# Kernel optimization log

Measured on AMD Instinct MI355X. Metric: run time of the kernel, lower is better.

The kernel has to match this reference:

```python
import jax, jax.numpy as jnp
import numpy as np

N_EMBED = 384
N_HEAD = 6
HEAD_DIM = N_EMBED // N_HEAD


def setup_inputs() -> dict:
    key = jax.random.key(0)
    k1, k2, k3 = jax.random.split(key, 3)
    B, T = 128, 256
    x = jax.random.normal(k1, (B, T, N_EMBED), dtype=jnp.float32)
    # nn.Linear(N_EMBED, 3*N_EMBED, bias=False): weight [3*N_EMBED, N_EMBED],
    # applied as x @ W.T -> store transposed [N_EMBED, 3*N_EMBED]
    W_qkv = jax.random.normal(k2, (N_EMBED, 3 * N_EMBED), dtype=jnp.float32) * (N_EMBED ** -0.5)
    W_proj = jax.random.normal(k3, (N_EMBED, N_EMBED), dtype=jnp.float32) * (N_EMBED ** -0.5)
    return {"x": x, "W_qkv": W_qkv, "W_proj": W_proj}


def reference(x, W_qkv, W_proj):
    B, T, C = x.shape
    qkv = jnp.einsum('btc,cd->btd', x, W_qkv)  # [B,T,3C]
    q, k, v = jnp.split(qkv, 3, axis=-1)
    # [B, H, T, Dh]
    q = q.reshape(B, T, N_HEAD, HEAD_DIM).transpose(0, 2, 1, 3)
    k = k.reshape(B, T, N_HEAD, HEAD_DIM).transpose(0, 2, 1, 3)
    v = v.reshape(B, T, N_HEAD, HEAD_DIM).transpose(0, 2, 1, 3)
    scale = HEAD_DIM ** -0.5
    wei = jnp.einsum('bhqd,bhkd->bhqk', q, k) * scale  # [B,H,T,T]
    causal = jnp.tril(jnp.ones((T, T), dtype=bool))
    wei = jnp.where(causal[None, None, :, :], wei, -jnp.inf)
    wei = jax.nn.softmax(wei, axis=-1)
    # dropout layers are identity in eval mode
    out = jnp.einsum('bhqk,bhkd->bhqd', wei, v)  # [B,H,T,Dh]
    out = out.transpose(0, 2, 1, 3).reshape(B, T, C)
    out = jnp.einsum('btc,cd->btd', out, W_proj)
    return out
```

## Files before the change

### kernel.cpp

```cpp
#include <hip/hip_runtime.h>
#include <hip/hip_bf16.h>

typedef __attribute__((ext_vector_type(8))) short short8;
typedef __attribute__((ext_vector_type(4))) float f32x4;
typedef __attribute__((ext_vector_type(4))) unsigned short ush4;

typedef const __attribute__((address_space(1))) void* gas_p;
typedef __attribute__((address_space(3))) void* las_p;
#define GLOAD_LDS16(g, l) __builtin_amdgcn_global_load_lds((gas_p)(const void*)(g), (las_p)(void*)(l), 16, 0, 0)

__device__ __forceinline__ unsigned short f2bf(float f) {
    union { float f; unsigned int u; } v; v.f = f;
    unsigned int r = v.u + 0x7FFFu + ((v.u >> 16) & 1u);
    return (unsigned short)(r >> 16);
}
__device__ __forceinline__ unsigned pk2(float a, float b) {
    return (unsigned)f2bf(a) | ((unsigned)f2bf(b) << 16);
}

__global__ __launch_bounds__(256) void cast_all_kernel(
    const float* __restrict__ x, const float* __restrict__ Wqkv, const float* __restrict__ Wproj,
    unsigned short* __restrict__ xb, unsigned short* __restrict__ wqkvt,
    unsigned short* __restrict__ wprojt)
{
    const int bid = blockIdx.x;
    if (bid < 6144) {
        int i = bid * 256 + threadIdx.x;
        const float4* p = (const float4*)x + (size_t)i * 2;
        float4 a = p[0], b = p[1];
        short8 o;
        o[0] = (short)f2bf(a.x); o[1] = (short)f2bf(a.y);
        o[2] = (short)f2bf(a.z); o[3] = (short)f2bf(a.w);
        o[4] = (short)f2bf(b.x); o[5] = (short)f2bf(b.y);
        o[6] = (short)f2bf(b.z); o[7] = (short)f2bf(b.w);
        *(short8*)(xb + (size_t)i * 8) = o;
    } else if (bid < 7872) {
        int idx = (bid - 6144) * 256 + threadIdx.x;
        int n = idx / 384, k = idx - n * 384;
        wqkvt[idx] = f2bf(Wqkv[(size_t)k * 1152 + n]);
    } else {
        int idx = (bid - 7872) * 256 + threadIdx.x;
        int n = idx / 384, k = idx - n * 384;
        wprojt[idx] = f2bf(Wproj[(size_t)k * 384 + n]);
    }
}

template<int MODE, int NP>
__global__ __launch_bounds__(256, 2) void gemm_bt_kernel(
    const unsigned short* __restrict__ A, const unsigned short* __restrict__ Bt,
    void* __restrict__ C0, unsigned short* __restrict__ C1,
    int M, int N, int K)
{
    __shared__ __align__(16) unsigned short Sh[3 * 128 * 64];
    unsigned short* As = Sh;
    const int tid = threadIdx.x;
    const int lane = tid & 63, wv = tid >> 6;
    const int c = lane & 15, g = lane >> 4;
    const int wm = (wv >> 1) * 64, wn = (wv & 1) * 64;

    const int mpx = (M >> 7) >> 3;
    const int id = blockIdx.x, xcd = id & 7, kk = id >> 3;
    const long m0 = (long)(xcd * mpx + kk / NP) * 128;
    const long n0 = (long)(kk % NP) * 128;

    f32x4 acc[4][4] = {};
    const int xr = (c & 7) << 4;

    int chrow[4], chsc[4];
    #pragma unroll
    for (int i = 0; i < 4; ++i) {
        int ch = i * 256 + wv * 64 + lane;
        chrow[i] = ch >> 3;
        chsc[i] = ((ch & 7) ^ (chrow[i] & 7)) * 8;
    }

#define STAGE_A(kt)                                                            \
    {                                                                          \
        _Pragma("unroll")                                                      \
        for (int i = 0; i < 4; ++i)                                            \
            GLOAD_LDS16(&A[(m0 + chrow[i]) * (size_t)K + (kt) + chsc[i]],      \
                        &As[(i * 256 + wv * 64) * 8]);                         \
    }
#define STAGE_B(bufofs, kt)                                                    \
    {                                                                          \
        _Pragma("unroll")                                                      \
        for (int i = 0; i < 4; ++i)                                            \
            GLOAD_LDS16(&Bt[(n0 + chrow[i]) * (size_t)K + (kt) + chsc[i]],     \
                        &Sh[(bufofs) + (i * 256 + wv * 64) * 8]);              \
    }

    STAGE_A(0);
    STAGE_B(8192, 0);
    __syncthreads();

    const int nt = K >> 6;
    for (int t = 0; t < nt; ++t) {
        const int bofs = 8192 + (t & 1) * 8192;
        if (t + 1 < nt) STAGE_B(8192 + ((t + 1) & 1) * 8192, (t + 1) * 64);
        const unsigned short* Bcur = Sh + bofs;
        #pragma unroll
        for (int ks = 0; ks < 2; ++ks) {
            short8 af[4], bf_[4];
            #pragma unroll
            for (int i = 0; i < 4; ++i)
                af[i] = *(const short8*)((char*)As +
                    (((wm + i * 16 + c) * 128 + (ks * 32 + g * 8) * 2) ^ xr));
            #pragma unroll
            for (int i = 0; i < 4; ++i)
                bf_[i] = *(const short8*)((char*)Bcur +
                    (((wn + i * 16 + c) * 128 + (ks * 32 + g * 8) * 2) ^ xr));
            #pragma unroll
            for (int mi = 0; mi < 4; ++mi)
                #pragma unroll
                for (int ni = 0; ni < 4; ++ni)
                    acc[mi][ni] = __builtin_amdgcn_mfma_f32_16x16x32_bf16(
                        af[mi], bf_[ni], acc[mi][ni], 0, 0, 0);
        }
        __syncthreads();
        if (t + 1 < nt) {
            STAGE_A((t + 1) * 64);
            __syncthreads();
        }
    }
#undef STAGE_A
#undef STAGE_B

    if (MODE == 1) {
        #pragma unroll
        for (int mi = 0; mi < 4; ++mi)
            #pragma unroll
            for (int ni = 0; ni < 4; ++ni)
                #pragma unroll
                for (int r = 0; r < 4; ++r) {
                    long m = m0 + wm + mi * 16 + g * 4 + r;
                    long n = n0 + wn + ni * 16 + c;
                    ((float*)C0)[m * N + n] = acc[mi][ni][r];
                }
    } else if (n0 < 768) {
        #pragma unroll
        for (int mi = 0; mi < 4; ++mi)
            #pragma unroll
            for (int ni = 0; ni < 4; ++ni)
                #pragma unroll
                for (int r = 0; r < 4; ++r) {
                    long m = m0 + wm + mi * 16 + g * 4 + r;
                    long n = n0 + wn + ni * 16 + c;
                    ((unsigned short*)C0)[m * 768 + n] = f2bf(acc[mi][ni][r]);
                }
    } else {
        char* wbase = (char*)Sh + wv * 8192;
        #pragma unroll
        for (int ni = 0; ni < 4; ++ni)
            #pragma unroll
            for (int mi = 0; mi < 4; ++mi)
                #pragma unroll
                for (int r = 0; r < 4; ++r) {
                    int d = ni * 16 + c, t = mi * 16 + g * 4 + r;
                    int byte = (d * 128 + t * 2) ^ ((d & 7) << 4);
                    *(unsigned short*)(wbase + byte) = f2bf(acc[mi][ni][r]);
                }
        __asm__ __volatile__("" ::: "memory");
        int h = (int)((n0 + wn - 768) >> 6);
        long b = (m0 + wm) >> 8;
        int t0 = (int)((m0 + wm) & 255);
        long bh = b * 6 + h;
        #pragma unroll
        for (int it = 0; it < 8; ++it) {
            int d = it * 8 + (lane >> 3), ck = lane & 7;
            short8 v = *(const short8*)(wbase + ((d * 128 + ck * 16) ^ ((d & 7) << 4)));
            *(short8*)&C1[(bh * 64 + d) * 256 + t0 + ck * 8] = v;
        }
    }
}

__global__ __launch_bounds__(256, 3) void attn_kernel(
    const unsigned short* __restrict__ qk,
    const unsigned short* __restrict__ vt,
    unsigned short* __restrict__ outp)
{
    const int bh = blockIdx.x;
    const int b = bh / 6, h = bh - b * 6;
    const int tid = threadIdx.x;
    const int lane = tid & 63, wv = tid >> 6;
    const int c = lane & 15, g = lane >> 4;

    __shared__ unsigned short Ks[256 * 64];
    __shared__ unsigned short Pl[4][16 * 64];

    #pragma unroll
    for (int it = 0; it < 8; ++it) {
        int ch = it * 256 + tid;
        int row = ch >> 3, col = (ch & 7) * 8;
        int db = (row * 128 + col * 2) ^ ((row & 7) << 4);
        *(short8*)((char*)Ks + db) =
            *(const short8*)&qk[(size_t)(b * 256 + row) * 768 + 384 + h * 64 + col];
    }
    __syncthreads();

    char* plw = (char*)Pl[wv];

    for (int t = 0; t < 2; ++t) {
        const int p = t ? 7 - wv : wv;
        const int jlast = p >> 1;
        const int modd = (p & 1) * 32;
        const int qt0 = p * 32;

        short8 aq[2][2];
        #pragma unroll
        for (int mi = 0; mi < 2; ++mi)
            #pragma unroll
            for (int ks = 0; ks < 2; ++ks)
                aq[mi][ks] = *(const short8*)&qk[
                    (size_t)(b * 256 + qt0 + mi * 16 + c) * 768 + h * 64 + ks * 32 + g * 8];

        f32x4 o[2][4] = {};
        float mrun[2] = {-1e30f, -1e30f}, lrun[2] = {0.f, 0.f};

        for (int j = 0; j <= jlast; ++j) {
            short8 bv[4][2];
            #pragma unroll
            for (int nd = 0; nd < 4; ++nd)
                #pragma unroll
                for (int ks = 0; ks < 2; ++ks)
                    bv[nd][ks] = *(const short8*)&vt[
                        ((size_t)bh * 64 + nd * 16 + c) * 256 + j * 64 + ks * 32 + g * 8];

            short8 bk[4][2];
            #pragma unroll
            for (int ni = 0; ni < 4; ++ni)
                #pragma unroll
                for (int ks = 0; ks < 2; ++ks) {
                    int key = j * 64 + ni * 16 + c;
                    bk[ni][ks] = *(const short8*)((char*)Ks +
                        ((key * 128 + (ks * 32 + g * 8) * 2) ^ ((key & 7) << 4)));
                }

            #pragma unroll
            for (int mi = 0; mi < 2; ++mi) {
                float pv[4][4];
                #pragma unroll
                for (int ni = 0; ni < 4; ++ni) {
                    f32x4 z = {0.f, 0.f, 0.f, 0.f};
                    z = __builtin_amdgcn_mfma_f32_16x16x32_bf16(bk[ni][0], aq[mi][0], z, 0, 0, 0);
                    z = __builtin_amdgcn_mfma_f32_16x16x32_bf16(bk[ni][1], aq[mi][1], z, 0, 0, 0);
                    #pragma unroll
                    for (int r = 0; r < 4; ++r) {
                        float v = z[r] * 0.125f;
                        if (j == jlast) {
                            int kloc = ni * 16 + g * 4 + r;
                            int qloc = mi * 16 + c + modd;
                            if (kloc > qloc) v = -1e30f;
                        }
                        pv[ni][r] = v;
                    }
                }
                float m01 = fmaxf(fmaxf(pv[0][0], pv[0][1]), fmaxf(pv[0][2], pv[0][3]));
                float m11 = fmaxf(fmaxf(pv[1][0], pv[1][1]), fmaxf(pv[1][2], pv[1][3]));
                float m21 = fmaxf(fmaxf(pv[2][0], pv[2][1]), fmaxf(pv[2][2], pv[2][3]));
                float m31 = fmaxf(fmaxf(pv[3][0], pv[3][1]), fmaxf(pv[3][2], pv[3][3]));
                float m1 = fmaxf(fmaxf(m01, m11), fmaxf(m21, m31));
                m1 = fmaxf(m1, __shfl_xor(m1, 16));
                m1 = fmaxf(m1, __shfl_xor(m1, 32));
                float mold = mrun[mi];
                float mnew = fmaxf(mold, m1);
                float fac = __expf(mold - mnew);
                float ssum = 0.f;
                #pragma unroll
                for (int ni = 0; ni < 4; ++ni)
                    #pragma unroll
                    for (int r = 0; r < 4; ++r) {
                        float pp = __expf(pv[ni][r] - mnew);
                        pv[ni][r] = pp;
                        ssum += pp;
                    }
                ssum += __shfl_xor(ssum, 16);
                ssum += __shfl_xor(ssum, 32);
                lrun[mi] = lrun[mi] * fac + ssum;
                mrun[mi] = mnew;
                #pragma unroll
                for (int nd = 0; nd < 4; ++nd)
                    #pragma unroll
                    for (int r = 0; r < 4; ++r) o[mi][nd][r] *= fac;

                __asm__ __volatile__("" ::: "memory");
                #pragma unroll
                for (int ni = 0; ni < 4; ++ni) {
                    uint2 w;
                    w.x = pk2(pv[ni][0], pv[ni][1]);
                    w.y = pk2(pv[ni][2], pv[ni][3]);
                    *(uint2*)(plw + ((c * 128 + ni * 32 + g * 8) ^ ((c & 7) << 4))) = w;
                }
                __asm__ __volatile__("" ::: "memory");

                short8 ap[2];
                #pragma unroll
                for (int ks = 0; ks < 2; ++ks)
                    ap[ks] = *(const short8*)(plw +
                        ((c * 128 + ks * 64 + g * 16) ^ ((c & 7) << 4)));

                #pragma unroll
                for (int nd = 0; nd < 4; ++nd) {
                    o[mi][nd] = __builtin_amdgcn_mfma_f32_16x16x32_bf16(bv[nd][0], ap[0], o[mi][nd], 0, 0, 0);
                    o[mi][nd] = __builtin_amdgcn_mfma_f32_16x16x32_bf16(bv[nd][1], ap[1], o[mi][nd], 0, 0, 0);
                }
                __asm__ __volatile__("" ::: "memory");
            }
        }

        #pragma unroll
        for (int mi = 0; mi < 2; ++mi) {
            float inv = 1.0f / lrun[mi];
            #pragma unroll
            for (int nd = 0; nd < 4; ++nd) {
                ush4 w;
                #pragma unroll
                for (int r = 0; r < 4; ++r) w[r] = f2bf(o[mi][nd][r] * inv);
                *(ush4*)&outp[((size_t)b * 256 + qt0 + mi * 16 + c) * 384 + h * 64 + nd * 16 + g * 4] = w;
            }
        }
    }
}

extern "C" void kernel_launch(void* const* d_in, const int* in_sizes, int n_in,
                              void* d_out, int out_size, void* d_ws, size_t ws_size,
                              hipStream_t stream) {
    const float* x     = (const float*)d_in[0];
    const float* Wqkv  = (const float*)d_in[1];
    const float* Wproj = (const float*)d_in[2];

    char* ws = (char*)d_ws;
    unsigned short* xb     = (unsigned short*)(ws);
    unsigned short* wqkvt  = (unsigned short*)(ws + 25165824);
    unsigned short* wprojt = (unsigned short*)(ws + 26050560);
    unsigned short* qkb    = (unsigned short*)(ws + 26345472);
    unsigned short* vtb    = (unsigned short*)(ws + 76677120);
    unsigned short* attnb  = (unsigned short*)(ws + 101842944);

    cast_all_kernel<<<8448, 256, 0, stream>>>(x, Wqkv, Wproj, xb, wqkvt, wprojt);

    gemm_bt_kernel<0, 9><<<2304, 256, 0, stream>>>(xb, wqkvt, (void*)qkb, vtb, 32768, 1152, 384);
    attn_kernel<<<768, 256, 0, stream>>>(qkb, vtb, attnb);
    gemm_bt_kernel<1, 3><<<768, 256, 0, stream>>>(attnb, wprojt, d_out, nullptr, 32768, 384, 384);
}
```

Measured before the change: 105.2 us.

## Load GEMM B operand directly from global and double-buffer A in LDS

The GEMM kernel no longer stages the B (transposed weight) tile through shared memory. Each wave now reads its B fragments straight from global memory into registers at the start of each k-tile, and A is double-buffered in LDS. This removes the second barrier per iteration and cuts LDS use from 48KB to 32KB, which may help occupancy. The cost is that B loads now have exposed global-memory latency right before the MFMAs, and waves sharing the same columns fetch the same data twice.

```diff
diff --git a/kernel.cpp b/kernel.cpp
--- a/kernel.cpp
+++ b/kernel.cpp
@@ -51,8 +51,7 @@
     void* __restrict__ C0, unsigned short* __restrict__ C1,
     int M, int N, int K)
 {
-    __shared__ __align__(16) unsigned short Sh[3 * 128 * 64];
-    unsigned short* As = Sh;
+    __shared__ __align__(16) unsigned short Sh[2 * 128 * 64];
     const int tid = threadIdx.x;
     const int lane = tid & 63, wv = tid >> 6;
     const int c = lane & 15, g = lane >> 4;
@@ -74,56 +73,47 @@
         chsc[i] = ((ch & 7) ^ (chrow[i] & 7)) * 8;
     }
 
-#define STAGE_A(kt)                                                            \
+#define STAGE_A(buf_shorts, kt)                                                \
     {                                                                          \
         _Pragma("unroll")                                                      \
         for (int i = 0; i < 4; ++i)                                            \
             GLOAD_LDS16(&A[(m0 + chrow[i]) * (size_t)K + (kt) + chsc[i]],      \
-                        &As[(i * 256 + wv * 64) * 8]);                         \
-    }
-#define STAGE_B(bufofs, kt)                                                    \
-    {                                                                          \
-        _Pragma("unroll")                                                      \
-        for (int i = 0; i < 4; ++i)                                            \
-            GLOAD_LDS16(&Bt[(n0 + chrow[i]) * (size_t)K + (kt) + chsc[i]],     \
-                        &Sh[(bufofs) + (i * 256 + wv * 64) * 8]);              \
-    }
-
-    STAGE_A(0);
-    STAGE_B(8192, 0);
+                        &Sh[(buf_shorts) + (i * 256 + wv * 64) * 8]);          \
+    }
+
+    STAGE_A(0, 0);
     __syncthreads();
 
     const int nt = K >> 6;
     for (int t = 0; t < nt; ++t) {
-        const int bofs = 8192 + (t & 1) * 8192;
-        if (t + 1 < nt) STAGE_B(8192 + ((t + 1) & 1) * 8192, (t + 1) * 64);
-        const unsigned short* Bcur = Sh + bofs;
+        const int curB = (t & 1) * 16384;
+        if (t + 1 < nt) STAGE_A(((t + 1) & 1) * 8192, (t + 1) * 64);
+
+        short8 bf_[2][4];
+        #pragma unroll
+        for (int ks = 0; ks < 2; ++ks)
+            #pragma unroll
+            for (int i = 0; i < 4; ++i)
+                bf_[ks][i] = *(const short8*)&Bt[
+                    (n0 + wn + i * 16 + c) * (size_t)K + t * 64 + ks * 32 + g * 8];
+
         #pragma unroll
         for (int ks = 0; ks < 2; ++ks) {
-            short8 af[4], bf_[4];
+            short8 af[4];
             #pragma unroll
             for (int i = 0; i < 4; ++i)
-                af[i] = *(const short8*)((char*)As +
+                af[i] = *(const short8*)((char*)Sh + curB +
                     (((wm + i * 16 + c) * 128 + (ks * 32 + g * 8) * 2) ^ xr));
-            #pragma unroll
-            for (int i = 0; i < 4; ++i)
-                bf_[i] = *(const short8*)((char*)Bcur +
-                    (((wn + i * 16 + c) * 128 + (ks * 32 + g * 8) * 2) ^ xr));
             #pragma unroll
             for (int mi = 0; mi < 4; ++mi)
                 #pragma unroll
                 for (int ni = 0; ni < 4; ++ni)
                     acc[mi][ni] = __builtin_amdgcn_mfma_f32_16x16x32_bf16(
-                        af[mi], bf_[ni], acc[mi][ni], 0, 0, 0);
+                        af[mi], bf_[ks][ni], acc[mi][ni], 0, 0, 0);
         }
         __syncthreads();
-        if (t + 1 < nt) {
-            STAGE_A((t + 1) * 64);
-            __syncthreads();
-        }
     }
 #undef STAGE_A
-#undef STAGE_B
 
     if (MODE == 1) {
         #pragma unroll
```

After: 142.6 us. 35.5% more time.
